# Kernel optimization log

Measured on AMD Instinct MI355X. Metric: run time of the kernel, lower is better.

Reference implementation:

```python
import jax, jax.numpy as jnp
import numpy as np
from jax.scipy.special import gammaln, logsumexp

# Model dims (match init_kwargs)
N1, N2, N3 = 16, 16, 8          # n_state_list
S = N1 * N2 * N3                # tot_dim = 2048 flattened states
M = 16                          # m_dimensions
T = 16384                       # T_max


def setup_inputs() -> dict:
    key = jax.random.key(0)
    ks = jax.random.split(key, 10)
    # observed Poisson counts, shape (T, M)
    x = jax.random.randint(ks[0], (T, M), 0, 20)
    # per-factor Poisson rates: lambda_list[i] = exp(randn(N_i, M)) as in __init__
    lam1 = jnp.exp(jax.random.normal(ks[1], (N1, M), dtype=jnp.float32))
    lam2 = jnp.exp(jax.random.normal(ks[2], (N2, M), dtype=jnp.float32))
    lam3 = jnp.exp(jax.random.normal(ks[3], (N3, M), dtype=jnp.float32))
    # per-factor log transition matrices: softmax over dim 0 (A[next, prev] columns sum to 1)
    logA1 = jax.nn.log_softmax(jax.random.normal(ks[4], (N1, N1), dtype=jnp.float32), axis=0)
    logA2 = jax.nn.log_softmax(jax.random.normal(ks[5], (N2, N2), dtype=jnp.float32), axis=0)
    logA3 = jax.nn.log_softmax(jax.random.normal(ks[6], (N3, N3), dtype=jnp.float32), axis=0)
    # per-factor log state priors: log_softmax(rand(N)*10)
    logpi1 = jax.nn.log_softmax(jax.random.uniform(ks[7], (N1,), dtype=jnp.float32) * 10.0)
    logpi2 = jax.nn.log_softmax(jax.random.uniform(ks[8], (N2,), dtype=jnp.float32) * 10.0)
    logpi3 = jax.nn.log_softmax(jax.random.uniform(ks[9], (N3,), dtype=jnp.float32) * 10.0)
    return {"x": x, "lam1": lam1, "lam2": lam2, "lam3": lam3,
            "logA1": logA1, "logA2": logA2, "logA3": logA3,
            "logpi1": logpi1, "logpi2": logpi2, "logpi3": logpi3}


def reference(x, lam1, lam2, lam3, logA1, logA2, logA3, logpi1, logpi2, logpi3):
    # combine_lambdas: lam_c[s1,s2,s3,m] = lam1[s1,m] + lam2[s2,m] + lam3[s3,m]
    lam_c = (lam1[:, None, None, :] + lam2[None, :, None, :]
             + lam3[None, None, :, :]).reshape(S, M)  # (S, M)
    xf = x.astype(jnp.float32)
    # Poisson log-pmf summed over the M observation dims:
    # em[t, s] = sum_m x[t,m]*log(lam_c[s,m]) - lam_c[s,m] - lgamma(x[t,m]+1)
    em = (xf @ jnp.log(lam_c).T
          - lam_c.sum(axis=-1)[None, :]
          - gammaln(xf + 1.0).sum(axis=-1)[:, None])  # (T, S)
    # combined log transition: logA[dest_flat, prev_flat] = sum_i logA_i[d_i, p_i]
    logA = (logA1[:, None, None, :, None, None]
            + logA2[None, :, None, None, :, None]
            + logA3[None, None, :, None, None, :]).reshape(S, S)
    # combined log priors
    logpi = (logpi1[:, None, None] + logpi2[None, :, None]
             + logpi3[None, None, :]).reshape(S)
    # log-domain forward recurrence (log_alpha_calc)
    alpha0 = em[0] + logpi
    def step(prev, em_t):
        a = em_t + logsumexp(logA + prev[None, :], axis=1)
        return a, None
    alpha_last, _ = jax.lax.scan(step, alpha0, em[1:])
    # log p(x) = logsumexp over final-step alpha
    return logsumexp(alpha_last)
```

## Files before the change

kernel.cpp:

```cpp
#include <hip/hip_runtime.h>
#include <math.h>

#define TMAX 16384
#define MDIM 16
#define SD   2048
#define CHK  1024
#define CLEN 16
#define WUP  16
#define EROWS 32

typedef unsigned int  uint;
typedef unsigned short ushort;
typedef __attribute__((ext_vector_type(8))) short short8;
typedef __attribute__((ext_vector_type(4))) short short4v;
typedef __attribute__((ext_vector_type(4))) float floatx4;
typedef __attribute__((ext_vector_type(2))) uint uintx2;

template<int CTRL>
__device__ __forceinline__ float fmax_dpp(float v) {
    int o = __builtin_amdgcn_update_dpp(__float_as_int(v), __float_as_int(v),
                                        CTRL, 0xf, 0xf, false);
    return fmaxf(v, __int_as_float(o));
}
__device__ __forceinline__ float waveMax64(float v) {
    v = fmax_dpp<0x111>(v);
    v = fmax_dpp<0x112>(v);
    v = fmax_dpp<0x114>(v);
    v = fmax_dpp<0x118>(v);
    v = fmax_dpp<0x142>(v);
    v = fmax_dpp<0x143>(v);
    return __int_as_float(__builtin_amdgcn_readlane(__float_as_int(v), 63));
}
__device__ __forceinline__ float waveSumF(float v) {
    #pragma unroll
    for (int o = 32; o > 0; o >>= 1) v += __shfl_xor(v, o, 64);
    return v;
}
__device__ __forceinline__ double waveSumD(double v) {
    #pragma unroll
    for (int o = 32; o > 0; o >>= 1) v += __shfl_xor(v, o, 64);
    return v;
}

__device__ __forceinline__ short f2bfs(float f) {
    uint u = __float_as_uint(f);
    return (short)((u + 0x7FFFu + ((u >> 16) & 1u)) >> 16);
}
__device__ __forceinline__ uint pkbf(float a, float b) {
    uint ua = __float_as_uint(a), ub = __float_as_uint(b);
    ua = (ua + 0x7FFFu + ((ua >> 16) & 1u)) >> 16;
    ub = (ub + 0x7FFFu + ((ub >> 16) & 1u)) & 0xFFFF0000u;
    return ua | ub;
}
__device__ __forceinline__ short4v pk4(float a, float b, float c, float d) {
    short4v r;
    r[0] = f2bfs(a); r[1] = f2bfs(b); r[2] = f2bfs(c); r[3] = f2bfs(d);
    return r;
}
__device__ __forceinline__ float bfl(uint u) { return __uint_as_float(u << 16); }
__device__ __forceinline__ float bfh(uint u) { return __uint_as_float(u & 0xFFFF0000u); }

#if __has_builtin(__builtin_amdgcn_mfma_f32_16x16x16bf16_1k)
#define MFMA16(a, b, c) __builtin_amdgcn_mfma_f32_16x16x16bf16_1k(a, b, c, 0, 0, 0)
#else
__device__ __forceinline__ floatx4 mfma16_asm(short4v a, short4v b, floatx4 c) {
    asm volatile("v_mfma_f32_16x16x16_bf16 %0, %1, %2, %0\n\t"
                 "s_nop 7\n\ts_nop 7"
                 : "+v"(c) : "v"(a), "v"(b));
    return c;
}
#define MFMA16(a, b, c) mfma16_asm(a, b, c)
#endif
#define MFMA32(a, b, c) __builtin_amdgcn_mfma_f32_16x16x32_bf16(a, b, c, 0, 0, 0)

__global__ __launch_bounds__(512, 2)
void emP_kernel(const int* __restrict__ x,
                const float* __restrict__ lam1,
                const float* __restrict__ lam2,
                const float* __restrict__ lam3,
                ushort* __restrict__ P,
                float* __restrict__ SumAuxArr,
                float* __restrict__ out) {
    __shared__ float wmx[EROWS][8];
    __shared__ float DemS[EROWS];
    __shared__ float lgtbl[32];
    __shared__ __align__(16) float xfs[EROWS * MDIM];
    __shared__ float lgred;
    const int tid = threadIdx.x, lane = tid & 63, wv = tid >> 6;
    const int q = lane >> 4, nn = lane & 15;
    const int d2 = 2 * wv + (nn >> 3);
    const int d3 = nn & 7;

    if (tid < 32) lgtbl[tid] = lgammaf((float)tid + 1.0f);
    if (tid == 0) lgred = 0.f;

    float llc[4][16], ls[4];
    #pragma unroll
    for (int j = 0; j < 4; ++j) {
        const int d1 = 4 * q + j;
        float sum = 0.f;
        #pragma unroll
        for (int m = 0; m < 16; ++m) {
            float la = lam1[d1 * 16 + m] + lam2[d2 * 16 + m] + lam3[d3 * 16 + m];
            sum += la;
            llc[j][m] = __logf(la);
        }
        ls[j] = sum;
    }

    const int t0 = blockIdx.x * EROWS;
    const int xv = x[t0 * MDIM + tid];
    xfs[tid] = (float)xv;
    __syncthreads();
    {
        double lg = (double)lgtbl[xv & 31];
        lg = waveSumD(lg);
        if (lane == 0) atomicAdd(&lgred, (float)lg);
    }

    float em[EROWS][4];
    #pragma unroll
    for (int ti = 0; ti < EROWS; ++ti) {
        float xr[16];
        *(float4*)&xr[0]  = *(const float4*)&xfs[ti * 16 + 0];
        *(float4*)&xr[4]  = *(const float4*)&xfs[ti * 16 + 4];
        *(float4*)&xr[8]  = *(const float4*)&xfs[ti * 16 + 8];
        *(float4*)&xr[12] = *(const float4*)&xfs[ti * 16 + 12];
        float vm = -3.4e38f;
        #pragma unroll
        for (int j = 0; j < 4; ++j) {
            float d = 0.f;
            #pragma unroll
            for (int m = 0; m < 16; ++m) d = fmaf(xr[m], llc[j][m], d);
            em[ti][j] = d - ls[j];
            vm = fmaxf(vm, em[ti][j]);
        }
        vm = waveMax64(vm);
        if (lane == 0) wmx[ti][wv] = vm;
    }
    __syncthreads();
    if (tid < 32) {
        float m = wmx[tid][0];
        #pragma unroll
        for (int i = 1; i < 8; ++i) m = fmaxf(m, wmx[tid][i]);
        DemS[tid] = m;
    }
    __syncthreads();

    #pragma unroll
    for (int ti = 0; ti < EROWS; ++ti) {
        const float Dem = DemS[ti];
        uint2 w;
        w.x = pkbf(__expf(em[ti][0] - Dem), __expf(em[ti][1] - Dem));
        w.y = pkbf(__expf(em[ti][2] - Dem), __expf(em[ti][3] - Dem));
        *(uint2*)(P + (size_t)(t0 + ti) * SD + tid * 4) = w;
    }

    if (tid == 0) {
        double sumD = 0.0;
        #pragma unroll
        for (int i = 0; i < EROWS; ++i) sumD += (double)DemS[i];
        SumAuxArr[blockIdx.x] = (float)sumD - lgred;
        if (blockIdx.x == 0) out[0] = 0.f;
    }
}

__global__ __launch_bounds__(512, 4)
void fhmm_chunk_kernel(const ushort* __restrict__ P,
                       const float* __restrict__ SumAuxArr,
                       const float* __restrict__ logA1,
                       const float* __restrict__ logA2,
                       const float* __restrict__ logA3,
                       const float* __restrict__ logpi1,
                       const float* __restrict__ logpi2,
                       const float* __restrict__ logpi3,
                       float* __restrict__ out)
{
    __shared__ __align__(16) short c1b[2 * 2048];
    __shared__ float wmA[8];
    __shared__ float sred[8];
    __shared__ float saux8[8];

    const int tid  = threadIdx.x;
    const int lane = tid & 63;
    const int wv   = tid >> 6;
    const int q    = lane >> 4;
    const int ml   = lane & 15;

    const int c    = blockIdx.x;
    const int tw0  = (c == 0) ? 0 : c * CLEN - WUP;
    const int tEnd = (c + 1) * CLEN;
    const int bAcc = c * CLEN;

    short4v bA1k;
    #pragma unroll
    for (int j = 0; j < 4; ++j)
        bA1k[j] = f2bfs(__expf(logA1[ml * 16 + 4 * q + j]));

    const int d2p = 2 * wv + (ml >> 3);
    const int d3p = ml & 7;
    short8 bK[4];
    #pragma unroll
    for (int jc = 0; jc < 4; ++jc)
        #pragma unroll
        for (int i = 0; i < 8; ++i)
            bK[jc][i] = f2bfs(__expf(logA2[d2p * 16 + 4 * jc + q] + logA3[d3p * 8 + i]));

    const int oS1w = ml * 128 + ((((2 * wv + (q >> 1)) ^ ml) & 15) << 3) + 4 * (q & 1);
    int o23[4];
    #pragma unroll
    for (int jc = 0; jc < 4; ++jc)
        o23[jc] = ml * 128 + ((((4 * jc + q) ^ ml) & 15) << 3);

    if (c == 0) {
        float sx = waveSumF(SumAuxArr[tid]);
        if (lane == 0) saux8[wv] = sx;
    }

    double OFF = 0.0;
    float nu0, nu1, nu2, nu3;
    {
        uintx2 p0 = *(const uintx2*)(P + (size_t)tw0 * SD + tid * 4);
        if (c == 0) {
            float lp23 = logpi2[d2p] + logpi3[d3p];
            nu0 = bfl(p0.x) * __expf(logpi1[4 * q + 0] + lp23);
            nu1 = bfh(p0.x) * __expf(logpi1[4 * q + 1] + lp23);
            nu2 = bfl(p0.y) * __expf(logpi1[4 * q + 2] + lp23);
            nu3 = bfh(p0.y) * __expf(logpi1[4 * q + 3] + lp23);
        } else {
            nu0 = bfl(p0.x); nu1 = bfh(p0.x);
            nu2 = bfl(p0.y); nu3 = bfh(p0.y);
        }
    }

    uintx2 Pb0 = *(const uintx2*)(P + (size_t)(tw0 + 1) * SD + tid * 4);
    uintx2 Pb1 = *(const uintx2*)(P + (size_t)(tw0 + 2) * SD + tid * 4);

#define FSTEP(T, RESC, ACCF)                                                    \
{                                                                               \
    const int par = (T) & 1;                                                    \
    short* c1cur = c1b + (par << 11);                                           \
    {                                               \
        short4v af = pk4(nu0, nu1, nu2, nu3);                                   \
        floatx4 s1 = {0.f, 0.f, 0.f, 0.f};                                      \
        s1 = MFMA16(af, bA1k, s1);                                              \
        ((uintx2*)(c1cur + oS1w))[0] =                                          \
            (uintx2){pkbf(s1[0], s1[1]), pkbf(s1[2], s1[3])};                   \
    }                                                                           \
    __syncthreads();                                                            \
    const int tn = ((T) + 2 < TMAX) ? (T) + 2 : TMAX - 1;                       \
    uintx2 Pb2 = *(const uintx2*)(P + (size_t)tn * SD + tid * 4);               \
    float inv = 1.f;                                                            \
    if (RESC) {                                                                 \
        float mp = waveMax64(wmA[lane & 7]);                                    \
        float mg = fmaxf(mp, 1e-30f);                                           \
        inv = __builtin_amdgcn_rcpf(mg);                                        \
        if ((ACCF) && tid == 0) OFF += (double)__logf(mg);                      \
    }                                                                           \
    {                                                      \
        floatx4 a0 = {0.f, 0.f, 0.f, 0.f};                                      \
        floatx4 a1 = {0.f, 0.f, 0.f, 0.f};                                      \
        a0 = MFMA32(*(const short8*)(c1cur + o23[0]), bK[0], a0);               \
        a1 = MFMA32(*(const short8*)(c1cur + o23[1]), bK[1], a1);               \
        a0 = MFMA32(*(const short8*)(c1cur + o23[2]), bK[2], a0);               \
        a1 = MFMA32(*(const short8*)(c1cur + o23[3]), bK[3], a1);               \
        floatx4 acc = a0 + a1;                                                  \
        if (RESC) {                                                             \
            nu0 = bfl(Pb0.x) * acc[0] * inv;                                    \
            nu1 = bfh(Pb0.x) * acc[1] * inv;                                    \
            nu2 = bfl(Pb0.y) * acc[2] * inv;                                    \
            nu3 = bfh(Pb0.y) * acc[3] * inv;                                    \
        } else {                                                                \
            nu0 = bfl(Pb0.x) * acc[0];                                          \
            nu1 = bfh(Pb0.x) * acc[1];                                          \
            nu2 = bfl(Pb0.y) * acc[2];                                          \
            nu3 = bfh(Pb0.y) * acc[3];                                          \
            float wa = waveMax64(fmaxf(fmaxf(nu0, nu1), fmaxf(nu2, nu3)));      \
            if (lane == 0) wmA[wv] = wa;                                        \
        }                                                                       \
    }                                                                           \
    Pb0 = Pb1; Pb1 = Pb2;                                                       \
}

    FSTEP(tw0 + 1, false, false);
    for (int te = tw0 + 2; te < tEnd; te += 2) {
        const bool accf = te > bAcc;
        FSTEP(te, true, accf);
        FSTEP(te + 1, false, false);
    }
#undef FSTEP

    __syncthreads();

    if (c == CHK - 1) {
        float su = waveSumF(nu0 + nu1 + nu2 + nu3);
        if (lane == 0) sred[wv] = su;
        __syncthreads();
        if (tid == 0) {
            float tot = 0.f;
            #pragma unroll
            for (int i = 0; i < 8; ++i) tot += sred[i];
            OFF += (double)__logf(tot);
            atomicAdd(out, (float)OFF);
        }
    } else {
        if (tid == 0) {
            float mp = wmA[0];
            #pragma unroll
            for (int i = 1; i < 8; ++i) mp = fmaxf(mp, wmA[i]);
            OFF += (double)__logf(fmaxf(mp, 1e-30f));
            if (c == 0) {
                float sa = 0.f;
                #pragma unroll
                for (int i = 0; i < 8; ++i) sa += saux8[i];
                OFF += (double)sa;
            }
            atomicAdd(out, (float)OFF);
        }
    }
}

extern "C" void kernel_launch(void* const* d_in, const int* in_sizes, int n_in,
                              void* d_out, int out_size, void* d_ws, size_t ws_size,
                              hipStream_t stream) {
    const int*   x      = (const int*)  d_in[0];
    const float* lam1   = (const float*)d_in[1];
    const float* lam2   = (const float*)d_in[2];
    const float* lam3   = (const float*)d_in[3];
    const float* logA1  = (const float*)d_in[4];
    const float* logA2  = (const float*)d_in[5];
    const float* logA3  = (const float*)d_in[6];
    const float* logpi1 = (const float*)d_in[7];
    const float* logpi2 = (const float*)d_in[8];
    const float* logpi3 = (const float*)d_in[9];
    float* out = (float*)d_out;

    float*  SumAuxArr = (float*)d_ws;
    ushort* P         = (ushort*)((char*)d_ws + 4096);

    emP_kernel <<<dim3(TMAX / EROWS), dim3(512), 0, stream>>>(
        x, lam1, lam2, lam3, P, SumAuxArr, out);
    fhmm_chunk_kernel<<<dim3(CHK), dim3(512), 0, stream>>>(
        P, SumAuxArr, logA1, logA2, logA3, logpi1, logpi2, logpi3, out);
}
```

Baseline: 159.1 us.

## Interleave two forward-recurrence chunks per block to share barriers and raise ILP

Each block now advances two independent chunk chains (A and B) in lockstep, with separate shared buffers and per-wave max arrays. Chain B's warm-up steps overlap chain A's accumulated range. The grid shrinks from 1024 to 512 blocks. The goal is to halve the number of block-wide barriers per unit of work and to hide MFMA and LDS latency by interleaving two independent dependency chains. The cost is higher register and LDS use per block and fewer blocks to spread across CUs.

```diff
diff --git a/kernel.cpp b/kernel.cpp
--- a/kernel.cpp
+++ b/kernel.cpp
@@ -4,9 +4,10 @@
 #define TMAX 16384
 #define MDIM 16
 #define SD   2048
-#define CHK  1024
 #define CLEN 16
 #define WUP  16
+#define CHKB 512
+#define NS   (CLEN + WUP - 1)
 #define EROWS 32
 
 typedef unsigned int  uint;
@@ -176,8 +177,9 @@
                        const float* __restrict__ logpi3,
                        float* __restrict__ out)
 {
-    __shared__ __align__(16) short c1b[2 * 2048];
-    __shared__ float wmA[8];
+    __shared__ __align__(16) short c1bA[2 * 2048];
+    __shared__ __align__(16) short c1bB[2 * 2048];
+    __shared__ float wmAA[8], wmAB[8];
     __shared__ float sred[8];
     __shared__ float saux8[8];
 
@@ -187,10 +189,9 @@
     const int q    = lane >> 4;
     const int ml   = lane & 15;
 
-    const int c    = blockIdx.x;
-    const int tw0  = (c == 0) ? 0 : c * CLEN - WUP;
-    const int tEnd = (c + 1) * CLEN;
-    const int bAcc = c * CLEN;
+    const int b   = blockIdx.x;
+    const int tA0 = (b == 0) ? 0 : 32 * b - 16;
+    const int tB0 = 32 * b;
 
     short4v bA1k;
     #pragma unroll
@@ -212,91 +213,135 @@
     for (int jc = 0; jc < 4; ++jc)
         o23[jc] = ml * 128 + ((((4 * jc + q) ^ ml) & 15) << 3);
 
-    if (c == 0) {
+    if (b == 0) {
         float sx = waveSumF(SumAuxArr[tid]);
         if (lane == 0) saux8[wv] = sx;
     }
 
     double OFF = 0.0;
-    float nu0, nu1, nu2, nu3;
+    float nuA[4], nuB[4];
     {
-        uintx2 p0 = *(const uintx2*)(P + (size_t)tw0 * SD + tid * 4);
-        if (c == 0) {
+        uintx2 p0 = *(const uintx2*)(P + (size_t)tA0 * SD + tid * 4);
+        if (b == 0) {
             float lp23 = logpi2[d2p] + logpi3[d3p];
-            nu0 = bfl(p0.x) * __expf(logpi1[4 * q + 0] + lp23);
-            nu1 = bfh(p0.x) * __expf(logpi1[4 * q + 1] + lp23);
-            nu2 = bfl(p0.y) * __expf(logpi1[4 * q + 2] + lp23);
-            nu3 = bfh(p0.y) * __expf(logpi1[4 * q + 3] + lp23);
+            nuA[0] = bfl(p0.x) * __expf(logpi1[4 * q + 0] + lp23);
+            nuA[1] = bfh(p0.x) * __expf(logpi1[4 * q + 1] + lp23);
+            nuA[2] = bfl(p0.y) * __expf(logpi1[4 * q + 2] + lp23);
+            nuA[3] = bfh(p0.y) * __expf(logpi1[4 * q + 3] + lp23);
         } else {
-            nu0 = bfl(p0.x); nu1 = bfh(p0.x);
-            nu2 = bfl(p0.y); nu3 = bfh(p0.y);
-        }
-    }
-
-    uintx2 Pb0 = *(const uintx2*)(P + (size_t)(tw0 + 1) * SD + tid * 4);
-    uintx2 Pb1 = *(const uintx2*)(P + (size_t)(tw0 + 2) * SD + tid * 4);
-
-#define FSTEP(T, RESC, ACCF)                                                    \
+            nuA[0] = bfl(p0.x); nuA[1] = bfh(p0.x);
+            nuA[2] = bfl(p0.y); nuA[3] = bfh(p0.y);
+        }
+    }
+    {
+        uintx2 p0 = *(const uintx2*)(P + (size_t)tB0 * SD + tid * 4);
+        nuB[0] = bfl(p0.x); nuB[1] = bfh(p0.x);
+        nuB[2] = bfl(p0.y); nuB[3] = bfh(p0.y);
+    }
+
+    uintx2 PbA0 = *(const uintx2*)(P + (size_t)(tA0 + 1) * SD + tid * 4);
+    uintx2 PbA1 = *(const uintx2*)(P + (size_t)(tA0 + 2) * SD + tid * 4);
+    uintx2 PbB0 = *(const uintx2*)(P + (size_t)(tB0 + 1) * SD + tid * 4);
+    uintx2 PbB1 = *(const uintx2*)(P + (size_t)(tB0 + 2) * SD + tid * 4);
+
+#define SSTEP(S, RESC, ACCFA, ACCFB)                                            \
 {                                                                               \
-    const int par = (T) & 1;                                                    \
-    short* c1cur = c1b + (par << 11);                                           \
-    {                                               \
-        short4v af = pk4(nu0, nu1, nu2, nu3);                                   \
-        floatx4 s1 = {0.f, 0.f, 0.f, 0.f};                                      \
-        s1 = MFMA16(af, bA1k, s1);                                              \
-        ((uintx2*)(c1cur + oS1w))[0] =                                          \
-            (uintx2){pkbf(s1[0], s1[1]), pkbf(s1[2], s1[3])};                   \
+    const int par = (S) & 1;          \
+    short* cAq = c1bA + (par << 11);                                            \
+    short* cBq = c1bB + (par << 11);                                            \
+    {                                 \
+        short4v afA = pk4(nuA[0], nuA[1], nuA[2], nuA[3]);                      \
+        short4v afB = pk4(nuB[0], nuB[1], nuB[2], nuB[3]);                      \
+        floatx4 sA = {0.f, 0.f, 0.f, 0.f};                                      \
+        floatx4 sB = {0.f, 0.f, 0.f, 0.f};                                      \
+        sA = MFMA16(afA, bA1k, sA);                                             \
+        sB = MFMA16(afB, bA1k, sB);                                             \
+        ((uintx2*)(cAq + oS1w))[0] = (uintx2){pkbf(sA[0], sA[1]), pkbf(sA[2], sA[3])}; \
+        ((uintx2*)(cBq + oS1w))[0] = (uintx2){pkbf(sB[0], sB[1]), pkbf(sB[2], sB[3])}; \
     }                                                                           \
     __syncthreads();                                                            \
-    const int tn = ((T) + 2 < TMAX) ? (T) + 2 : TMAX - 1;                       \
-    uintx2 Pb2 = *(const uintx2*)(P + (size_t)tn * SD + tid * 4);               \
-    float inv = 1.f;                                                            \
+    const int tnA = (tA0 + (S) + 2 < TMAX) ? tA0 + (S) + 2 : TMAX - 1;          \
+    const int tnB = (tB0 + (S) + 2 < TMAX) ? tB0 + (S) + 2 : TMAX - 1;          \
+    uintx2 PbA2 = *(const uintx2*)(P + (size_t)tnA * SD + tid * 4);             \
+    uintx2 PbB2 = *(const uintx2*)(P + (size_t)tnB * SD + tid * 4);             \
+    float invA = 1.f, invB = 1.f;                                               \
     if (RESC) {                                                                 \
-        float mp = waveMax64(wmA[lane & 7]);                                    \
-        float mg = fmaxf(mp, 1e-30f);                                           \
-        inv = __builtin_amdgcn_rcpf(mg);                                        \
-        if ((ACCF) && tid == 0) OFF += (double)__logf(mg);                      \
-    }                                                                           \
-    {                                                      \
-        floatx4 a0 = {0.f, 0.f, 0.f, 0.f};                                      \
-        floatx4 a1 = {0.f, 0.f, 0.f, 0.f};                                      \
-        a0 = MFMA32(*(const short8*)(c1cur + o23[0]), bK[0], a0);               \
-        a1 = MFMA32(*(const short8*)(c1cur + o23[1]), bK[1], a1);               \
-        a0 = MFMA32(*(const short8*)(c1cur + o23[2]), bK[2], a0);               \
-        a1 = MFMA32(*(const short8*)(c1cur + o23[3]), bK[3], a1);               \
-        floatx4 acc = a0 + a1;                                                  \
-        if (RESC) {                                                             \
-            nu0 = bfl(Pb0.x) * acc[0] * inv;                                    \
-            nu1 = bfh(Pb0.x) * acc[1] * inv;                                    \
-            nu2 = bfl(Pb0.y) * acc[2] * inv;                                    \
-            nu3 = bfh(Pb0.y) * acc[3] * inv;                                    \
-        } else {                                                                \
-            nu0 = bfl(Pb0.x) * acc[0];                                          \
-            nu1 = bfh(Pb0.x) * acc[1];                                          \
-            nu2 = bfl(Pb0.y) * acc[2];                                          \
-            nu3 = bfh(Pb0.y) * acc[3];                                          \
-            float wa = waveMax64(fmaxf(fmaxf(nu0, nu1), fmaxf(nu2, nu3)));      \
-            if (lane == 0) wmA[wv] = wa;                                        \
+        float mpA = waveMax64(wmAA[lane & 7]);                                  \
+        float mpB = waveMax64(wmAB[lane & 7]);                                  \
+        float mgA = fmaxf(mpA, 1e-30f);                                         \
+        float mgB = fmaxf(mpB, 1e-30f);                                         \
+        invA = __builtin_amdgcn_rcpf(mgA);                                      \
+        invB = __builtin_amdgcn_rcpf(mgB);                                      \
+        if (tid == 0) {                                                         \
+            if (ACCFA) OFF += (double)__logf(mgA);                              \
+            if (ACCFB) OFF += (double)__logf(mgB);                              \
         }                                                                       \
     }                                                                           \
-    Pb0 = Pb1; Pb1 = Pb2;                                                       \
-}
-
-    FSTEP(tw0 + 1, false, false);
-    for (int te = tw0 + 2; te < tEnd; te += 2) {
-        const bool accf = te > bAcc;
-        FSTEP(te, true, accf);
-        FSTEP(te + 1, false, false);
-    }
-#undef FSTEP
+    {              \
+        short8 fA0 = *(const short8*)(cAq + o23[0]);                            \
+        short8 fA1 = *(const short8*)(cAq + o23[1]);                            \
+        short8 fA2 = *(const short8*)(cAq + o23[2]);                            \
+        short8 fA3 = *(const short8*)(cAq + o23[3]);                            \
+        short8 fB0 = *(const short8*)(cBq + o23[0]);                            \
+        short8 fB1 = *(const short8*)(cBq + o23[1]);                            \
+        short8 fB2 = *(const short8*)(cBq + o23[2]);                            \
+        short8 fB3 = *(const short8*)(cBq + o23[3]);                            \
+        floatx4 aA0 = {0.f, 0.f, 0.f, 0.f};                                     \
+        floatx4 aA1 = {0.f, 0.f, 0.f, 0.f};                                     \
+        floatx4 aB0 = {0.f, 0.f, 0.f, 0.f};                                     \
+        floatx4 aB1 = {0.f, 0.f, 0.f, 0.f};                                     \
+        aA0 = MFMA32(fA0, bK[0], aA0);  aB0 = MFMA32(fB0, bK[0], aB0);          \
+        aA1 = MFMA32(fA1, bK[1], aA1);  aB1 = MFMA32(fB1, bK[1], aB1);          \
+        aA0 = MFMA32(fA2, bK[2], aA0);  aB0 = MFMA32(fB2, bK[2], aB0);          \
+        aA1 = MFMA32(fA3, bK[3], aA1);  aB1 = MFMA32(fB3, bK[3], aB1);          \
+        floatx4 accA = aA0 + aA1;                                               \
+        floatx4 accB = aB0 + aB1;                                               \
+        if (RESC) {                                                             \
+            nuA[0] = bfl(PbA0.x) * accA[0] * invA;                              \
+            nuA[1] = bfh(PbA0.x) * accA[1] * invA;                              \
+            nuA[2] = bfl(PbA0.y) * accA[2] * invA;                              \
+            nuA[3] = bfh(PbA0.y) * accA[3] * invA;                              \
+            nuB[0] = bfl(PbB0.x) * accB[0] * invB;                              \
+            nuB[1] = bfh(PbB0.x) * accB[1] * invB;                              \
+            nuB[2] = bfl(PbB0.y) * accB[2] * invB;                              \
+            nuB[3] = bfh(PbB0.y) * accB[3] * invB;                              \
+        } else {                                                                \
+            nuA[0] = bfl(PbA0.x) * accA[0];                                     \
+            nuA[1] = bfh(PbA0.x) * accA[1];                                     \
+            nuA[2] = bfl(PbA0.y) * accA[2];                                     \
+            nuA[3] = bfh(PbA0.y) * accA[3];                                     \
+            nuB[0] = bfl(PbB0.x) * accB[0];                                     \
+            nuB[1] = bfh(PbB0.x) * accB[1];                                     \
+            nuB[2] = bfl(PbB0.y) * accB[2];                                     \
+            nuB[3] = bfh(PbB0.y) * accB[3];                                     \
+            float waA = waveMax64(fmaxf(fmaxf(nuA[0], nuA[1]), fmaxf(nuA[2], nuA[3]))); \
+            float waB = waveMax64(fmaxf(fmaxf(nuB[0], nuB[1]), fmaxf(nuB[2], nuB[3]))); \
+            if (lane == 0) { wmAA[wv] = waA; wmAB[wv] = waB; }                  \
+        }                                                                       \
+    }                                                                           \
+    PbA0 = PbA1; PbA1 = PbA2; PbB0 = PbB1; PbB1 = PbB2;                         \
+}
+
+    SSTEP(1, false, false, false);
+    for (int s = 2; s < NS; s += 2) {
+        const bool accfA = (b == 0) || (s > WUP);
+        const bool accfB = (s > WUP);
+        SSTEP(s, true, accfA, accfB);
+        SSTEP(s + 1, false, false, false);
+    }
+#undef SSTEP
 
     __syncthreads();
 
-    if (c == CHK - 1) {
-        float su = waveSumF(nu0 + nu1 + nu2 + nu3);
+    if (b == CHKB - 1) {
+        float su = waveSumF(nuB[0] + nuB[1] + nuB[2] + nuB[3]);
         if (lane == 0) sred[wv] = su;
         __syncthreads();
         if (tid == 0) {
+            float mpA = wmAA[0];
+            #pragma unroll
+            for (int i = 1; i < 8; ++i) mpA = fmaxf(mpA, wmAA[i]);
+            OFF += (double)__logf(fmaxf(mpA, 1e-30f));
             float tot = 0.f;
             #pragma unroll
             for (int i = 0; i < 8; ++i) tot += sred[i];
@@ -305,11 +350,15 @@
         }
     } else {
         if (tid == 0) {
-            float mp = wmA[0];
+            float mpA = wmAA[0], mpB = wmAB[0];
             #pragma unroll
-            for (int i = 1; i < 8; ++i) mp = fmaxf(mp, wmA[i]);
-            OFF += (double)__logf(fmaxf(mp, 1e-30f));
-            if (c == 0) {
+            for (int i = 1; i < 8; ++i) {
+                mpA = fmaxf(mpA, wmAA[i]);
+                mpB = fmaxf(mpB, wmAB[i]);
+            }
+            OFF += (double)__logf(fmaxf(mpA, 1e-30f));
+            OFF += (double)__logf(fmaxf(mpB, 1e-30f));
+            if (b == 0) {
                 float sa = 0.f;
                 #pragma unroll
                 for (int i = 0; i < 8; ++i) sa += saux8[i];
@@ -340,6 +389,6 @@
 
     emP_kernel <<<dim3(TMAX / EROWS), dim3(512), 0, stream>>>(
         x, lam1, lam2, lam3, P, SumAuxArr, out);
-    fhmm_chunk_kernel<<<dim3(CHK), dim3(512), 0, stream>>>(
+    fhmm_chunk_kernel<<<dim3(CHKB), dim3(512), 0, stream>>>(
         P, SumAuxArr, logA1, logA2, logA3, logpi1, logpi2, logpi3, out);
 }
```

New measurement: 156.2 us. No clear change (-1.8%).
